# Kernel optimization log

Hardware: AMD Instinct MI355X
Metric: run time of the kernel (lower is better)

## Reference

```python
import jax, jax.numpy as jnp
import numpy as np

WINDOW_SIZE = 3
SIGMA = 1.5
C1 = 0.01 ** 2
C2 = 0.03 ** 2


def gaussian_window(channel, window_size=WINDOW_SIZE, sigma=SIGMA):
    x = jnp.arange(window_size, dtype=jnp.float32) - window_size // 2
    g1 = jnp.exp(-(x ** 2) / (2.0 * sigma ** 2))
    g1 = g1 / g1.sum()
    g2 = jnp.outer(g1, g1)  # [k, k]
    # depthwise kernel OIHW: [C, 1, k, k]
    return jnp.broadcast_to(g2, (channel, 1, window_size, window_size))


def depthwise_conv(x, window, channel, window_size=WINDOW_SIZE):
    pad = window_size // 2
    return jax.lax.conv_general_dilated(
        x, window,
        window_strides=(1, 1),
        padding=((pad, pad), (pad, pad)),
        dimension_numbers=('NCHW', 'OIHW', 'NCHW'),
        feature_group_count=channel,
    )


def setup_inputs() -> dict:
    key = jax.random.key(0)
    k1, k2 = jax.random.split(key)
    img1 = jax.random.uniform(k1, (32, 3, 512, 512), dtype=jnp.float32)
    img2 = jax.random.uniform(k2, (32, 3, 512, 512), dtype=jnp.float32)
    return {"img1": img1, "img2": img2}


def reference(img1, img2):
    channel = img1.shape[1]
    window = gaussian_window(channel)

    mu1 = depthwise_conv(img1, window, channel)
    mu2 = depthwise_conv(img2, window, channel)
    mu1_sq = mu1 * mu1
    mu2_sq = mu2 * mu2
    mu1_mu2 = mu1 * mu2

    sigma1_sq = depthwise_conv(img1 * img1, window, channel) - mu1_sq
    sigma2_sq = depthwise_conv(img2 * img2, window, channel) - mu2_sq
    sigma12 = depthwise_conv(img1 * img2, window, channel) - mu1_mu2

    ssim_map = ((2.0 * mu1_mu2 + C1) * (2.0 * sigma12 + C2)) / (
        (mu1_sq + mu2_sq + C1) * (sigma1_sq + sigma2_sq + C2))

    # size_sum defaults to True inside ssim() -> scalar sum
    return 1.0 - ssim_map.sum()
```

## Files before the change

kernel.cpp:

```cpp
#include <hip/hip_runtime.h>

#define IMG_H 512
#define IMG_W 512
#define RH 16
#define STRIPS (IMG_H / RH)
#define QWAVES 4
#define PLANE_N (IMG_H * IMG_W)

constexpr float W_E = 0.30780133f;
constexpr float W_C = 0.38439734f;
constexpr float C1v = 1e-4f;
constexpr float C2v = 9e-4f;

struct HRow { float h1[2], h2[2], h11[2], h22[2], h12[2]; };
struct Raw { float2 a, b; float aE, bE; };

__device__ __forceinline__ void load_row(const float* __restrict__ A,
                                         const float* __restrict__ B,
                                         int row, int col0, int ecol, Raw& r) {
    if ((unsigned)row < (unsigned)IMG_H) {
        const size_t off = (size_t)row * IMG_W;
        r.a = *(const float2*)(A + off + col0);
        r.b = *(const float2*)(B + off + col0);
        float ae = 0.f, be = 0.f;
        if (ecol >= 0) {
            ae = A[off + ecol];
            be = B[off + ecol];
        }
        r.aE = ae; r.bE = be;
    } else {
        r.a = make_float2(0.f, 0.f);
        r.b = make_float2(0.f, 0.f);
        r.aE = 0.f; r.bE = 0.f;
    }
}

__device__ __forceinline__ void compute_h(const Raw& r, int lane, HRow& H) {
    float aL = __shfl_up(r.a.y, 1);
    float bL = __shfl_up(r.b.y, 1);
    float aR = __shfl_down(r.a.x, 1);
    float bR = __shfl_down(r.b.x, 1);
    if (lane == 0)  { aL = r.aE; bL = r.bE; }
    if (lane == 63) { aR = r.aE; bR = r.bE; }
    const float av[4] = {aL, r.a.x, r.a.y, aR};
    const float bv[4] = {bL, r.b.x, r.b.y, bR};
#pragma unroll
    for (int c = 0; c < 2; ++c) {
        const float am = av[c], a0 = av[c + 1], ap = av[c + 2];
        const float bm = bv[c], b0 = bv[c + 1], bp = bv[c + 2];
        H.h1[c]  = fmaf(W_E, am + ap, W_C * a0);
        H.h2[c]  = fmaf(W_E, bm + bp, W_C * b0);
        H.h11[c] = fmaf(W_E, fmaf(am, am, ap * ap), W_C * (a0 * a0));
        H.h22[c] = fmaf(W_E, fmaf(bm, bm, bp * bp), W_C * (b0 * b0));
        H.h12[c] = fmaf(W_E, fmaf(am, bm, ap * bp), W_C * (a0 * b0));
    }
}

__device__ __forceinline__ float out_row(const HRow& P, const HRow& Q,
                                         const HRow& R) {
    float s = 0.f;
#pragma unroll
    for (int c = 0; c < 2; ++c) {
        const float m1  = fmaf(W_E, P.h1[c]  + R.h1[c],  W_C * Q.h1[c]);
        const float m2  = fmaf(W_E, P.h2[c]  + R.h2[c],  W_C * Q.h2[c]);
        const float e11 = fmaf(W_E, P.h11[c] + R.h11[c], W_C * Q.h11[c]);
        const float e22 = fmaf(W_E, P.h22[c] + R.h22[c], W_C * Q.h22[c]);
        const float e12 = fmaf(W_E, P.h12[c] + R.h12[c], W_C * Q.h12[c]);
        const float mu1s = m1 * m1, mu2s = m2 * m2, m12 = m1 * m2;
        const float s11 = e11 - mu1s, s22 = e22 - mu2s, s12 = e12 - m12;
        const float num = fmaf(2.f, m12, C1v) * fmaf(2.f, s12, C2v);
        const float den = (mu1s + mu2s + C1v) * (s11 + s22 + C2v);
        s = fmaf(num, __builtin_amdgcn_rcpf(den), s);
    }
    return s;
}

__global__ __launch_bounds__(256)
void ssim_main_kernel(const float* __restrict__ img1,
                      const float* __restrict__ img2,
                      float* __restrict__ wsum)
{
    const int t = threadIdx.x;
    const int lane = t & 63;
    const int task = blockIdx.x * 4 + (t >> 6);
    const int quar  = task & (QWAVES - 1);
    const int strip = (task >> 2) & (STRIPS - 1);
    const int plane = task >> 7;
    const int y0 = strip * RH;
    const int col0 = quar * 128 + (lane << 1);
    const float* __restrict__ A = img1 + (size_t)plane * PLANE_N;
    const float* __restrict__ B = img2 + (size_t)plane * PLANE_N;

    int ecol = -1;
    if (lane == 0 && col0 > 0) ecol = col0 - 1;
    if (lane == 63 && col0 + 2 < IMG_W) ecol = col0 + 2;

    HRow HA, HB, HC;
    Raw R0, R1;
    float tsum = 0.f;

#define STANZA(Hm2, Hm1, Hnew, RU, RL, yload, doout)        \
    do {                                                    \
        load_row(A, B, (yload), col0, ecol, (RL));          \
        compute_h((RU), lane, (Hnew));                      \
        if (doout) tsum += out_row((Hm2), (Hm1), (Hnew));   \
        __builtin_amdgcn_sched_barrier(0);                  \
    } while (0)

    load_row(A, B, y0 - 1, col0, ecol, R0);
    STANZA(HA, HA, HA, R0, R1, y0,     false);
    STANZA(HA, HA, HB, R1, R0, y0 + 1, false);

#pragma unroll 1
    for (int g = 0; g < 2; ++g) {
        const int yb = y0 + 2 + 6 * g;
        STANZA(HA, HB, HC, R0, R1, yb,     true);
        STANZA(HB, HC, HA, R1, R0, yb + 1, true);
        STANZA(HC, HA, HB, R0, R1, yb + 2, true);
        STANZA(HA, HB, HC, R1, R0, yb + 3, true);
        STANZA(HB, HC, HA, R0, R1, yb + 4, true);
        STANZA(HC, HA, HB, R1, R0, yb + 5, true);
    }
    STANZA(HA, HB, HC, R0, R1, y0 + 14, true);
    STANZA(HB, HC, HA, R1, R0, y0 + 15, true);
    STANZA(HC, HA, HB, R0, R1, y0 + 16, true);
    STANZA(HA, HB, HC, R1, R0, -1,      true);
#undef STANZA

#pragma unroll
    for (int off = 32; off; off >>= 1) tsum += __shfl_xor(tsum, off, 64);
    if (lane == 0) wsum[task] = tsum;
}

__global__ __launch_bounds__(256) void ssim_fin_kernel(
    const float* __restrict__ wsum, float* __restrict__ out, int n)
{
    const int t = threadIdx.x;
    double s = 0.0;
    for (int i = t; i < n; i += 256) s += (double)wsum[i];
#pragma unroll
    for (int off = 32; off; off >>= 1) s += __shfl_xor(s, off, 64);
    __shared__ double wp[4];
    if ((t & 63) == 0) wp[t >> 6] = s;
    __syncthreads();
    if (t == 0) out[0] = 1.0f - (float)(wp[0] + wp[1] + wp[2] + wp[3]);
}

extern "C" void kernel_launch(void* const* d_in, const int* in_sizes, int n_in,
                              void* d_out, int out_size, void* d_ws, size_t ws_size,
                              hipStream_t stream) {
    const float* img1 = (const float*)d_in[0];
    const float* img2 = (const float*)d_in[1];
    float* out = (float*)d_out;
    float* wsum = (float*)d_ws;

    const int planes = in_sizes[0] / PLANE_N;
    const int tasks = planes * STRIPS * QWAVES;
    const int blocks = tasks / 4;

    ssim_main_kernel<<<blocks, 256, 0, stream>>>(img1, img2, wsum);
    ssim_fin_kernel<<<1, 256, 0, stream>>>(wsum, out, tasks);
}
```

Baseline: 229.1 us.

## Rescale Gaussian weights, packed v2f math, and rolling vertical accumulators

```diff
diff --git a/kernel.cpp b/kernel.cpp
--- a/kernel.cpp
+++ b/kernel.cpp
@@ -7,21 +7,22 @@
 #define QWAVES 4
 #define PLANE_N (IMG_H * IMG_W)
 
-constexpr float W_E = 0.30780133f;
-constexpr float W_C = 0.38439734f;
-constexpr float C1v = 1e-4f;
-constexpr float C2v = 9e-4f;
+typedef float v2f __attribute__((ext_vector_type(2)));
 
-struct HRow { float h1[2], h2[2], h11[2], h22[2], h12[2]; };
-struct Raw { float2 a, b; float aE, bE; };
+constexpr float RW  = 0.80073744f;
+constexpr float KK  = 0.14776133f;
+constexpr float C1N = 4.58013e-3f;
+constexpr float C2N = 6.09091e-3f;
+
+struct Raw { v2f a, b; float aE, bE; };
 
 __device__ __forceinline__ void load_row(const float* __restrict__ A,
                                          const float* __restrict__ B,
                                          int row, int col0, int ecol, Raw& r) {
     if ((unsigned)row < (unsigned)IMG_H) {
         const size_t off = (size_t)row * IMG_W;
-        r.a = *(const float2*)(A + off + col0);
-        r.b = *(const float2*)(B + off + col0);
+        r.a = *(const v2f*)(A + off + col0);
+        r.b = *(const v2f*)(B + off + col0);
         float ae = 0.f, be = 0.f;
         if (ecol >= 0) {
             ae = A[off + ecol];
@@ -29,50 +30,31 @@
         }
         r.aE = ae; r.bE = be;
     } else {
-        r.a = make_float2(0.f, 0.f);
-        r.b = make_float2(0.f, 0.f);
+        r.a = (v2f){0.f, 0.f};
+        r.b = (v2f){0.f, 0.f};
         r.aE = 0.f; r.bE = 0.f;
     }
 }
 
-__device__ __forceinline__ void compute_h(const Raw& r, int lane, HRow& H) {
-    float aL = __shfl_up(r.a.y, 1);
-    float bL = __shfl_up(r.b.y, 1);
-    float aR = __shfl_down(r.a.x, 1);
-    float bR = __shfl_down(r.b.x, 1);
-    if (lane == 0)  { aL = r.aE; bL = r.bE; }
-    if (lane == 63) { aR = r.aE; bR = r.bE; }
-    const float av[4] = {aL, r.a.x, r.a.y, aR};
-    const float bv[4] = {bL, r.b.x, r.b.y, bR};
-#pragma unroll
-    for (int c = 0; c < 2; ++c) {
-        const float am = av[c], a0 = av[c + 1], ap = av[c + 2];
-        const float bm = bv[c], b0 = bv[c + 1], bp = bv[c + 2];
-        H.h1[c]  = fmaf(W_E, am + ap, W_C * a0);
-        H.h2[c]  = fmaf(W_E, bm + bp, W_C * b0);
-        H.h11[c] = fmaf(W_E, fmaf(am, am, ap * ap), W_C * (a0 * a0));
-        H.h22[c] = fmaf(W_E, fmaf(bm, bm, bp * bp), W_C * (b0 * b0));
-        H.h12[c] = fmaf(W_E, fmaf(am, bm, ap * bp), W_C * (a0 * b0));
-    }
-}
+struct HV { v2f h1, h2, h11, h22, h12; };
 
-__device__ __forceinline__ float out_row(const HRow& P, const HRow& Q,
-                                         const HRow& R) {
-    float s = 0.f;
-#pragma unroll
-    for (int c = 0; c < 2; ++c) {
-        const float m1  = fmaf(W_E, P.h1[c]  + R.h1[c],  W_C * Q.h1[c]);
-        const float m2  = fmaf(W_E, P.h2[c]  + R.h2[c],  W_C * Q.h2[c]);
-        const float e11 = fmaf(W_E, P.h11[c] + R.h11[c], W_C * Q.h11[c]);
-        const float e22 = fmaf(W_E, P.h22[c] + R.h22[c], W_C * Q.h22[c]);
-        const float e12 = fmaf(W_E, P.h12[c] + R.h12[c], W_C * Q.h12[c]);
-        const float mu1s = m1 * m1, mu2s = m2 * m2, m12 = m1 * m2;
-        const float s11 = e11 - mu1s, s22 = e22 - mu2s, s12 = e12 - m12;
-        const float num = fmaf(2.f, m12, C1v) * fmaf(2.f, s12, C2v);
-        const float den = (mu1s + mu2s + C1v) * (s11 + s22 + C2v);
-        s = fmaf(num, __builtin_amdgcn_rcpf(den), s);
-    }
-    return s;
+__device__ __forceinline__ void compute_h(const Raw& r, bool lane0, bool lane63,
+                                          HV& H) {
+    const float ax = r.a.x, ay = r.a.y, bx = r.b.x, by = r.b.y;
+    float aL = __shfl_up(ay, 1);
+    float bL = __shfl_up(by, 1);
+    float aR = __shfl_down(ax, 1);
+    float bR = __shfl_down(bx, 1);
+    if (lane0)  { aL = r.aE; bL = r.bE; }
+    if (lane63) { aR = r.aE; bR = r.bE; }
+    const float aL2 = aL*aL, ax2 = ax*ax, ay2 = ay*ay, aR2 = aR*aR;
+    const float bL2 = bL*bL, bx2 = bx*bx, by2 = by*by, bR2 = bR*bR;
+    const float abL = aL*bL, abx = ax*bx, aby = ay*by, abR = aR*bR;
+    H.h1  = (v2f){fmaf(RW, aL  + ay,  ax),  fmaf(RW, ax  + aR,  ay)};
+    H.h2  = (v2f){fmaf(RW, bL  + by,  bx),  fmaf(RW, bx  + bR,  by)};
+    H.h11 = (v2f){fmaf(RW, aL2 + ay2, ax2), fmaf(RW, ax2 + aR2, ay2)};
+    H.h22 = (v2f){fmaf(RW, bL2 + by2, bx2), fmaf(RW, bx2 + bR2, by2)};
+    H.h12 = (v2f){fmaf(RW, abL + aby, abx), fmaf(RW, abx + abR, aby)};
 }
 
 __global__ __launch_bounds__(256)
@@ -88,48 +70,84 @@
     const int plane = task >> 7;
     const int y0 = strip * RH;
     const int col0 = quar * 128 + (lane << 1);
+    const bool lane0 = (lane == 0), lane63 = (lane == 63);
     const float* __restrict__ A = img1 + (size_t)plane * PLANE_N;
     const float* __restrict__ B = img2 + (size_t)plane * PLANE_N;
 
     int ecol = -1;
-    if (lane == 0 && col0 > 0) ecol = col0 - 1;
-    if (lane == 63 && col0 + 2 < IMG_W) ecol = col0 + 2;
+    if (lane0  && col0 > 0) ecol = col0 - 1;
+    if (lane63 && col0 + 2 < IMG_W) ecol = col0 + 2;
 
-    HRow HA, HB, HC;
-    Raw R0, R1;
-    float tsum = 0.f;
+    const v2f RWv = {RW, RW};
+    const v2f TWO = {2.f, 2.f};
+    const v2f MKK = {-KK, -KK};
+    const v2f C1v = {C1N, C1N};
+    const v2f C2v = {C2N, C2N};
 
-#define STANZA(Hm2, Hm1, Hnew, RU, RL, yload, doout)        \
-    do {                                                    \
-        load_row(A, B, (yload), col0, ecol, (RL));          \
-        compute_h((RU), lane, (Hnew));                      \
-        if (doout) tsum += out_row((Hm2), (Hm1), (Hnew));   \
-        __builtin_amdgcn_sched_barrier(0);                  \
+    v2f ac0_1 = {0,0}, ac1_1 = {0,0}, ac0_2 = {0,0}, ac1_2 = {0,0};
+    v2f ac0_11 = {0,0}, ac1_11 = {0,0}, ac0_22 = {0,0}, ac1_22 = {0,0};
+    v2f ac0_12 = {0,0}, ac1_12 = {0,0};
+    v2f vsum = {0.f, 0.f};
+
+    Raw R0, R1, R2;
+    load_row(A, B, y0 - 1, col0, ecol, R0);
+    load_row(A, B, y0,     col0, ecol, R1);
+
+#define VF(a, b, c) __builtin_elementwise_fma((a), (b), (c))
+#define STANZA(RU, RL, k, DOOUT, DOLOAD)                                    \
+    do {                                                                    \
+        if (DOLOAD) load_row(A, B, y0 + 1 + (k), col0, ecol, RL);           \
+        HV H;                                                               \
+        compute_h((RU), lane0, lane63, H);                                  \
+        if (DOOUT) {                                                        \
+            const v2f M1  = VF(RWv, H.h1,  ac0_1);                          \
+            const v2f M2  = VF(RWv, H.h2,  ac0_2);                          \
+            const v2f E11 = VF(RWv, H.h11, ac0_11);                         \
+            const v2f E22 = VF(RWv, H.h22, ac0_22);                         \
+            const v2f E12 = VF(RWv, H.h12, ac0_12);                         \
+            const v2f m12 = M1 * M2;                                        \
+            const v2f p   = VF(M2, M2, M1 * M1);                            \
+            const v2f num1 = VF(TWO, m12, C1v);                             \
+            const v2f s12  = VF(MKK, m12, E12);                             \
+            const v2f num2 = VF(TWO, s12, C2v);                             \
+            const v2f den1 = p + C1v;                                       \
+            const v2f tt   = E11 + E22;                                     \
+            const v2f sp   = VF(MKK, p, tt);                                \
+            const v2f den2 = sp + C2v;                                      \
+            const v2f num  = num1 * num2;                                   \
+            const v2f den  = den1 * den2;                                   \
+            const v2f rv = {__builtin_amdgcn_rcpf(den.x),                   \
+                            __builtin_amdgcn_rcpf(den.y)};                  \
+            vsum = VF(num, rv, vsum);                                       \
+        }                                                                   \
+        ac0_1  = ac1_1  + H.h1;   ac1_1  = RWv * H.h1;                      \
+        ac0_2  = ac1_2  + H.h2;   ac1_2  = RWv * H.h2;                      \
+        ac0_11 = ac1_11 + H.h11;  ac1_11 = RWv * H.h11;                     \
+        ac0_22 = ac1_22 + H.h22;  ac1_22 = RWv * H.h22;                     \
+        ac0_12 = ac1_12 + H.h12;  ac1_12 = RWv * H.h12;                     \
+        __builtin_amdgcn_sched_barrier(0);                                  \
     } while (0)
 
-    load_row(A, B, y0 - 1, col0, ecol, R0);
-    STANZA(HA, HA, HA, R0, R1, y0,     false);
-    STANZA(HA, HA, HB, R1, R0, y0 + 1, false);
+    STANZA(R0, R2, 0, false, true);
+    STANZA(R1, R0, 1, false, true);
+    STANZA(R2, R1, 2, true,  true);
+#pragma unroll
+    for (int g = 1; g <= 4; ++g) {
+        const int k = 3 * g;
+        STANZA(R0, R2, k,     true, true);
+        STANZA(R1, R0, k + 1, true, true);
+        STANZA(R2, R1, k + 2, true, true);
+    }
+    STANZA(R0, R2, 15, true, true);
+    STANZA(R1, R0, 16, true, false);
+    STANZA(R2, R1, 17, true, false);
+#undef STANZA
+#undef VF
 
-#pragma unroll 1
-    for (int g = 0; g < 2; ++g) {
-        const int yb = y0 + 2 + 6 * g;
-        STANZA(HA, HB, HC, R0, R1, yb,     true);
-        STANZA(HB, HC, HA, R1, R0, yb + 1, true);
-        STANZA(HC, HA, HB, R0, R1, yb + 2, true);
-        STANZA(HA, HB, HC, R1, R0, yb + 3, true);
-        STANZA(HB, HC, HA, R0, R1, yb + 4, true);
-        STANZA(HC, HA, HB, R1, R0, yb + 5, true);
-    }
-    STANZA(HA, HB, HC, R0, R1, y0 + 14, true);
-    STANZA(HB, HC, HA, R1, R0, y0 + 15, true);
-    STANZA(HC, HA, HB, R0, R1, y0 + 16, true);
-    STANZA(HA, HB, HC, R1, R0, -1,      true);
-#undef STANZA
-
+    float tsum = vsum.x + vsum.y;
 #pragma unroll
     for (int off = 32; off; off >>= 1) tsum += __shfl_xor(tsum, off, 64);
-    if (lane == 0) wsum[task] = tsum;
+    if (lane0) wsum[task] = tsum;
 }
 
 __global__ __launch_bounds__(256) void ssim_fin_kernel(
```

New measurement: 231.7 us. Within noise of the previous version (+1.1%).
